# Performance work log

Hardware: AMD Instinct MI355X
Metric: run time of the kernel (lower is better)

Reference implementation:

```python
import jax, jax.numpy as jnp
import numpy as np

S, E, H, D, F = 2048, 1280, 16, 80, 5120
EPS = 1e-6


def _ln(x, g, b):
    m = x.mean(-1, keepdims=True)
    v = x.var(-1, keepdims=True)
    return (x - m) * jax.lax.rsqrt(v + EPS) * g + b


def _rotate_half(x):
    x1, x2 = jnp.split(x, 2, axis=-1)
    return jnp.concatenate([-x2, x1], axis=-1)


def _quick_gelu(x):
    return x * jax.nn.sigmoid(1.702 * x)


def setup_inputs() -> dict:
    key = jax.random.key(0)
    ks = jax.random.split(key, 12)
    inp = {
        "hidden_states": jax.random.normal(ks[0], (S, E), jnp.float32),
        "attention_mask": jnp.ones((1, 1, S, S), jnp.bool_),
        "cos": jax.random.uniform(ks[1], (S, D), jnp.float32),
        "sin": jax.random.uniform(ks[2], (S, D), jnp.float32),
        "ln1_g": jnp.ones((E,), jnp.float32),
        "ln1_b": jnp.zeros((E,), jnp.float32),
        "ln2_g": jnp.ones((E,), jnp.float32),
        "ln2_b": jnp.zeros((E,), jnp.float32),
        "w_qkv": jax.random.normal(ks[3], (E, 3 * E), jnp.float32) * (E ** -0.5),
        "b_qkv": jax.random.normal(ks[4], (3 * E,), jnp.float32) * 0.02,
        "w_o": jax.random.normal(ks[5], (E, E), jnp.float32) * (E ** -0.5),
        "b_o": jax.random.normal(ks[6], (E,), jnp.float32) * 0.02,
        "w_fc1": jax.random.normal(ks[7], (E, F), jnp.float32) * (E ** -0.5),
        "b_fc1": jax.random.normal(ks[8], (F,), jnp.float32) * 0.02,
        "w_fc2": jax.random.normal(ks[9], (F, E), jnp.float32) * (F ** -0.5),
        "b_fc2": jax.random.normal(ks[10], (E,), jnp.float32) * 0.02,
    }
    return inp


def reference(hidden_states, attention_mask, cos, sin, ln1_g, ln1_b, ln2_g, ln2_b,
              w_qkv, b_qkv, w_o, b_o, w_fc1, b_fc1, w_fc2, b_fc2):
    x = hidden_states  # [S, E]
    h = _ln(x, ln1_g, ln1_b)
    qkv = h @ w_qkv + b_qkv  # [S, 3E]
    q, k, v = jnp.split(qkv, 3, axis=-1)
    q = q.reshape(S, H, D)
    k = k.reshape(S, H, D)
    v = v.reshape(S, H, D)
    # rotary in fp32, cos/sin broadcast over head axis: [S, 1, D]
    c = cos[:, None, :].astype(jnp.float32)
    s = sin[:, None, :].astype(jnp.float32)
    qf, kf = q.astype(jnp.float32), k.astype(jnp.float32)
    q = (qf * c + _rotate_half(qf) * s).astype(q.dtype)
    k = (kf * c + _rotate_half(kf) * s).astype(k.dtype)
    # attention scores [H, S, S]
    scores = jnp.einsum('shd,thd->hst', q, k) / np.float32(np.sqrt(D))
    scores = jnp.where(attention_mask[0], scores, jnp.finfo(scores.dtype).min)
    probs = jax.nn.softmax(scores.astype(jnp.float32), axis=-1).astype(q.dtype)
    attn = jnp.einsum('hst,thd->shd', probs, v).reshape(S, E)
    attn = attn @ w_o + b_o
    x = x + attn
    h2 = _ln(x, ln2_g, ln2_b)
    mlp = _quick_gelu(h2 @ w_fc1 + b_fc1) @ w_fc2 + b_fc2
    return x + mlp
```

## Files before the change

kernel.cpp:

```cpp
#include <hip/hip_runtime.h>
#include <stdint.h>
#include <math.h>

#define S_LEN 2048
#define EMB   1280
#define NHEAD 16
#define HDIM  80
#define FDIM  5120

typedef __bf16 bf16x8 __attribute__((ext_vector_type(8)));
typedef float  f32x4  __attribute__((ext_vector_type(4)));
typedef int    i32x4  __attribute__((ext_vector_type(4)));
typedef unsigned short u16x8 __attribute__((ext_vector_type(8)));
typedef unsigned short u16x4 __attribute__((ext_vector_type(4)));

__device__ __forceinline__ float b2f(unsigned short u) {
    union { float f; unsigned int i; } x; x.i = ((unsigned int)u) << 16; return x.f;
}
__device__ __forceinline__ unsigned short f2b(float f) {
    union { float f; unsigned int i; } x; x.f = f;
    unsigned int r = x.i + 0x7FFFu + ((x.i >> 16) & 1u);
    return (unsigned short)(r >> 16);
}

__device__ __forceinline__ float wave_rsum(float v) {
    #pragma unroll
    for (int o = 32; o; o >>= 1) v += __shfl_down(v, o);
    return v;
}

typedef const __attribute__((address_space(1))) unsigned int* as1_u32p;
typedef __attribute__((address_space(3))) unsigned int* as3_u32p;
__device__ __forceinline__ void gload16(const unsigned short* g, unsigned short* l) {
    __builtin_amdgcn_global_load_lds((as1_u32p)g, (as3_u32p)l, 16, 0, 0);
}

__global__ __launch_bounds__(256) void transpose_conv_kernel(
    const float* __restrict__ in, unsigned short* __restrict__ out,
    int R, int C)
{
    __shared__ unsigned short tile[64][65];
    int c0 = blockIdx.x * 64, r0 = blockIdx.y * 64;
    int tx = threadIdx.x & 63, ty = threadIdx.x >> 6;
    #pragma unroll
    for (int j = 0; j < 16; ++j) {
        int row = ty + j * 4;
        tile[row][tx] = f2b(in[(size_t)(r0 + row) * C + c0 + tx]);
    }
    __syncthreads();
    #pragma unroll
    for (int j = 0; j < 16; ++j) {
        int row = ty + j * 4;
        out[(size_t)(c0 + row) * R + r0 + tx] = tile[tx][row];
    }
}

__global__ __launch_bounds__(256) void ln_kernel(
    const float* __restrict__ x,
    const float* __restrict__ g,
    const float* __restrict__ b,
    unsigned short* __restrict__ out)
{
    int row = blockIdx.x, tid = threadIdx.x;
    int lane = tid & 63, wave = tid >> 6;
    const float* xr = x + (size_t)row * EMB;
    float v[5], s = 0.f, ss = 0.f;
    #pragma unroll
    for (int i = 0; i < 5; ++i) {
        float f = xr[tid + i * 256];
        v[i] = f; s += f; ss += f * f;
    }
    s = wave_rsum(s); ss = wave_rsum(ss);
    __shared__ float rs[4], rss[4];
    if (lane == 0) { rs[wave] = s; rss[wave] = ss; }
    __syncthreads();
    float st  = rs[0] + rs[1] + rs[2] + rs[3];
    float sst = rss[0] + rss[1] + rss[2] + rss[3];
    float mean = st * (1.0f / EMB);
    float var  = sst * (1.0f / EMB) - mean * mean;
    float inv  = rsqrtf(var + 1e-6f);
    unsigned short* orow = out + (size_t)row * EMB;
    #pragma unroll
    for (int i = 0; i < 5; ++i) {
        int c = tid + i * 256;
        orow[c] = f2b((v[i] - mean) * inv * g[c] + b[c]);
    }
}

template<int EPI, int OM, int NT, int SPLIT>
__global__ __launch_bounds__(256) void gemm_kernel(
    const unsigned short* __restrict__ A,
    const unsigned short* __restrict__ Bt,
    const float* __restrict__ bias,
    const float* __restrict__ res,
    void* __restrict__ Cv,
    int M, int N, int K)
{
    __shared__ __align__(16) unsigned short As[128 * 32];
    __shared__ __align__(16) unsigned short Bs[NT * 32 * 32];

    int tid = threadIdx.x;
    int lane = tid & 63, wave = tid >> 6;
    int m0 = blockIdx.x * 128, n0 = blockIdx.y * (NT * 32);
    int wm = (wave >> 1) * 64, wn = (wave & 1) * (NT * 16);
    int kc = K / SPLIT;
    int kbeg = blockIdx.z * kc;

    f32x4 acc[4][NT];
    #pragma unroll
    for (int i = 0; i < 4; ++i)
        #pragma unroll
        for (int j = 0; j < NT; ++j)
            acc[i][j] = (f32x4){0.f, 0.f, 0.f, 0.f};

    int srow = tid >> 2;
    int scol = (tid & 3) * 8;
    const unsigned short* Ap0 = A  + (size_t)(m0 + srow) * K + scol + kbeg;
    const unsigned short* Ap1 = Ap0 + (size_t)64 * K;
    const unsigned short* Bp0 = Bt + (size_t)(n0 + srow) * K + scol + kbeg;
    const unsigned short* Bp1 = Bp0 + (size_t)64 * K;
    unsigned short* Asw0 = &As[srow * 32 + scol];
    unsigned short* Asw1 = &As[(srow + 64) * 32 + scol];
    unsigned short* Bsw0 = &Bs[srow * 32 + scol];
    unsigned short* Bsw1 = &Bs[(srow + 64) * 32 + scol];

    int arow = lane & 15, aq = (lane >> 4) * 8;
    int aoff[4], boff[NT];
    #pragma unroll
    for (int i = 0; i < 4; ++i)
        aoff[i] = (wm + i * 16 + arow) * 32 + aq;
    #pragma unroll
    for (int i = 0; i < NT; ++i)
        boff[i] = (wn + i * 16 + arow) * 32 + aq;

    for (int k0 = 0; k0 < kc; k0 += 32) {
        __syncthreads();
        gload16(Ap0 + k0, Asw0);
        gload16(Ap1 + k0, Asw1);
        gload16(Bp0 + k0, Bsw0);
        if (NT == 4) gload16(Bp1 + k0, Bsw1);
        __syncthreads();

        bf16x8 af[4], bfm[NT];
        #pragma unroll
        for (int i = 0; i < 4; ++i)
            af[i] = *(const bf16x8*)&As[aoff[i]];
        #pragma unroll
        for (int i = 0; i < NT; ++i)
            bfm[i] = *(const bf16x8*)&Bs[boff[i]];
        #pragma unroll
        for (int mi = 0; mi < 4; ++mi)
            #pragma unroll
            for (int ni = 0; ni < NT; ++ni)
                acc[mi][ni] = __builtin_amdgcn_mfma_f32_16x16x32_bf16(
                    af[mi], bfm[ni], acc[mi][ni], 0, 0, 0);
    }

    int col = lane & 15;
    int rbase = (lane >> 4) * 4;
    #pragma unroll
    for (int ni = 0; ni < NT; ++ni) {
        int gn = n0 + wn + ni * 16 + col;
        float bv = (OM == 2) ? 0.f : bias[gn];
        #pragma unroll
        for (int mi = 0; mi < 4; ++mi) {
            int gm = m0 + wm + mi * 16 + rbase;
            #pragma unroll
            for (int r = 0; r < 4; ++r) {
                float v = acc[mi][ni][r] + bv;
                if (OM != 2) {
                    if (EPI == 1) v = v / (1.0f + expf(-1.702f * v));
                    if (EPI == 2) v += res[(size_t)(gm + r) * N + gn];
                }
                if (OM == 2)
                    ((float*)Cv)[((size_t)blockIdx.z * M + gm + r) * N + gn] = v;
                else if (OM == 1)
                    ((float*)Cv)[(size_t)(gm + r) * N + gn] = v;
                else
                    ((unsigned short*)Cv)[(size_t)(gm + r) * N + gn] = f2b(v);
            }
        }
    }
}

__global__ __launch_bounds__(256) void reduce4_kernel(
    const float* __restrict__ part,
    const float* __restrict__ res,
    const float* __restrict__ bias,
    float* __restrict__ out)
{
    size_t i4 = ((size_t)blockIdx.x * 256 + threadIdx.x) * 4;
    int colb = (int)(i4 % EMB);
    f32x4 a = *(const f32x4*)&res[i4];
    f32x4 bv = *(const f32x4*)&bias[colb];
    a += bv;
    const size_t slice = (size_t)S_LEN * EMB;
    #pragma unroll
    for (int z = 0; z < 4; ++z)
        a += *(const f32x4*)&part[z * slice + i4];
    *(f32x4*)&out[i4] = a;
}

__global__ __launch_bounds__(128) void rope_kernel(
    const unsigned short* __restrict__ qkv,
    const float* __restrict__ cosb,
    const float* __restrict__ sinb,
    unsigned short* __restrict__ q_out,
    unsigned short* __restrict__ k_out)
{
    int bs = blockIdx.x;
    int s = bs / NHEAD, h = bs % NHEAD;
    int d = threadIdx.x;
    if (d >= HDIM) return;
    const unsigned short* base = qkv + (size_t)s * (3 * EMB) + h * HDIM;
    int partner = (d < 40) ? d + 40 : d - 40;
    float sgn = (d < 40) ? -1.f : 1.f;
    float qv = b2f(base[d]);
    float kv = b2f(base[EMB + d]);
    float qr = b2f(base[partner]) * sgn;
    float kr = b2f(base[EMB + partner]) * sgn;
    float c  = cosb[s * HDIM + d];
    float sn = sinb[s * HDIM + d];
    size_t o = ((size_t)h * S_LEN + s) * HDIM + d;
    q_out[o] = f2b(qv * c + qr * sn);
    k_out[o] = f2b(kv * c + kr * sn);
}

__global__ __launch_bounds__(256) void vtrans_kernel(
    const unsigned short* __restrict__ qkv,
    unsigned short* __restrict__ vt)
{
    __shared__ unsigned short t[64 * 84];
    int h = blockIdx.x >> 5, stile = blockIdx.x & 31;
    int s0 = stile * 64;
    int tid = threadIdx.x;
    #pragma unroll
    for (int i = 0; i < 5; ++i) {
        int u = tid + i * 256;
        int row = u / 20, col = (u % 20) * 4;
        *(u16x4*)&t[row * 84 + col] =
            *(const u16x4*)(qkv + (size_t)(s0 + row) * (3 * EMB) + 2 * EMB + h * HDIM + col);
    }
    __syncthreads();
    #pragma unroll
    for (int i = 0; i < 5; ++i) {
        int w = tid + i * 256;
        int d = w >> 4, c4 = (w & 15) * 4;
        u16x4 pk;
        #pragma unroll
        for (int j = 0; j < 4; ++j) pk[j] = t[(c4 + j) * 84 + d];
        *(u16x4*)(vt + ((size_t)h * HDIM + d) * S_LEN + s0 + c4) = pk;
    }
}

__global__ __launch_bounds__(256) void fattn_kernel(
    const unsigned short* __restrict__ q,
    const unsigned short* __restrict__ k,
    const unsigned short* __restrict__ vt,
    unsigned short* __restrict__ out)
{
    __shared__ __align__(16) unsigned short Qs[64 * 96];
    __shared__ __align__(16) unsigned short Ks[64 * 96];
    __shared__ __align__(16) unsigned short Vs[80 * 72];
    __shared__ __align__(16) unsigned short Pt[4 * 16 * 72];

    int tid = threadIdx.x;
    int lane = tid & 63, wave = tid >> 6;
    int arow = lane & 15, quad = lane >> 4;
    int h = blockIdx.x >> 5, qb = blockIdx.x & 31;
    int s0 = qb * 64;
    const float c = 0.16129856f;

    const unsigned short* qbase = q + ((size_t)h * S_LEN + s0) * HDIM;
    const unsigned short* kbase = k + (size_t)h * S_LEN * HDIM;
    const unsigned short* vbase = vt + (size_t)h * HDIM * S_LEN;

    #pragma unroll
    for (int i = 0; i < 5; ++i) {
        int u = tid + i * 256;
        int row = u / 20, col = (u % 20) * 4;
        *(u16x4*)&Qs[row * 96 + col] = *(const u16x4*)(qbase + u * 4);
    }
    {
        int zr = tid >> 2, zc = 80 + (tid & 3) * 4;
        *(u16x4*)&Qs[zr * 96 + zc] = (u16x4){0, 0, 0, 0};
        *(u16x4*)&Ks[zr * 96 + zc] = (u16x4){0, 0, 0, 0};
    }

    int pw = wave * 16 * 72;
    float m_run = -3e38f;
    float l_run = 0.f;
    f32x4 o[5];
    #pragma unroll
    for (int di = 0; di < 5; ++di) o[di] = (f32x4){0.f, 0.f, 0.f, 0.f};

    for (int it = 0; it < S_LEN / 64; ++it) {
        int t0 = it * 64;
        u16x4 kreg[5], vreg[5];
        #pragma unroll
        for (int i = 0; i < 5; ++i) {
            int u = tid + i * 256;
            kreg[i] = *(const u16x4*)(kbase + (size_t)t0 * HDIM + u * 4);
            int vrow = u >> 4, vc4 = (u & 15) * 4;
            vreg[i] = *(const u16x4*)(vbase + (size_t)vrow * S_LEN + t0 + vc4);
        }
        __syncthreads();
        #pragma unroll
        for (int i = 0; i < 5; ++i) {
            int u = tid + i * 256;
            *(u16x4*)&Ks[(u / 20) * 96 + (u % 20) * 4] = kreg[i];
            *(u16x4*)&Vs[(u >> 4) * 72 + (u & 15) * 4] = vreg[i];
        }
        __syncthreads();

        f32x4 sc[4];
        #pragma unroll
        for (int ni = 0; ni < 4; ++ni) sc[ni] = (f32x4){0.f, 0.f, 0.f, 0.f};
        #pragma unroll
        for (int kk = 0; kk < 3; ++kk) {
            bf16x8 bq = *(const bf16x8*)&Qs[(wave * 16 + arow) * 96 + kk * 32 + quad * 8];
            #pragma unroll
            for (int ni = 0; ni < 4; ++ni) {
                bf16x8 ak = *(const bf16x8*)&Ks[(ni * 16 + arow) * 96 + kk * 32 + quad * 8];
                sc[ni] = __builtin_amdgcn_mfma_f32_16x16x32_bf16(ak, bq, sc[ni], 0, 0, 0);
            }
        }

        float tm = -3e38f;
        #pragma unroll
        for (int ni = 0; ni < 4; ++ni)
            #pragma unroll
            for (int r = 0; r < 4; ++r) tm = fmaxf(tm, sc[ni][r]);
        tm = fmaxf(tm, __shfl_xor(tm, 16));
        tm = fmaxf(tm, __shfl_xor(tm, 32));
        float mn = fmaxf(m_run, tm);
        float alpha = exp2f((m_run - mn) * c);
        m_run = mn;
        float mc = mn * c;
        float rs = 0.f;
        #pragma unroll
        for (int ni = 0; ni < 4; ++ni) {
            #pragma unroll
            for (int r = 0; r < 4; ++r) {
                float p = exp2f(sc[ni][r] * c - mc);
                sc[ni][r] = p;
                rs += p;
            }
        }
        rs += __shfl_xor(rs, 16);
        rs += __shfl_xor(rs, 32);
        l_run = l_run * alpha + rs;

        #pragma unroll
        for (int ni = 0; ni < 4; ++ni) {
            u16x4 pk;
            #pragma unroll
            for (int r = 0; r < 4; ++r) {
                __bf16 pb = (__bf16)sc[ni][r];
                pk[r] = *(unsigned short*)&pb;
            }
            *(u16x4*)&Pt[pw + arow * 72 + ni * 16 + quad * 4] = pk;
        }

        float al[4];
        #pragma unroll
        for (int r = 0; r < 4; ++r)
            al[r] = __shfl(alpha, (lane & 48) | (quad * 4 + r));
        #pragma unroll
        for (int di = 0; di < 5; ++di)
            #pragma unroll
            for (int r = 0; r < 4; ++r) o[di][r] *= al[r];

        #pragma unroll
        for (int kk = 0; kk < 2; ++kk) {
            bf16x8 ap = *(const bf16x8*)&Pt[pw + arow * 72 + kk * 32 + quad * 8];
            #pragma unroll
            for (int di = 0; di < 5; ++di) {
                bf16x8 bv = *(const bf16x8*)&Vs[(di * 16 + arow) * 72 + kk * 32 + quad * 8];
                o[di] = __builtin_amdgcn_mfma_f32_16x16x32_bf16(ap, bv, o[di], 0, 0, 0);
            }
        }
    }

    float inv[4];
    #pragma unroll
    for (int r = 0; r < 4; ++r)
        inv[r] = 1.f / __shfl(l_run, (lane & 48) | (quad * 4 + r));
    #pragma unroll
    for (int r = 0; r < 4; ++r) {
        int gq = s0 + wave * 16 + quad * 4 + r;
        unsigned short* op = out + (size_t)gq * EMB + h * HDIM;
        #pragma unroll
        for (int di = 0; di < 5; ++di)
            op[di * 16 + arow] = f2b(o[di][r] * inv[r]);
    }
}

extern "C" void kernel_launch(void* const* d_in, const int* in_sizes, int n_in,
                              void* d_out, int out_size, void* d_ws, size_t ws_size,
                              hipStream_t stream)
{
    const float* hidden = (const float*)d_in[0];
    const float* cosb  = (const float*)d_in[2];
    const float* sinb  = (const float*)d_in[3];
    const float* ln1g  = (const float*)d_in[4];
    const float* ln1b  = (const float*)d_in[5];
    const float* ln2g  = (const float*)d_in[6];
    const float* ln2b  = (const float*)d_in[7];
    const float* w_qkv = (const float*)d_in[8];
    const float* b_qkv = (const float*)d_in[9];
    const float* w_o   = (const float*)d_in[10];
    const float* b_o   = (const float*)d_in[11];
    const float* w_fc1 = (const float*)d_in[12];
    const float* b_fc1 = (const float*)d_in[13];
    const float* w_fc2 = (const float*)d_in[14];
    const float* b_fc2 = (const float*)d_in[15];

    char* ws = (char*)d_ws;
    size_t off = 0;
    auto alloc = [&](size_t bytes) -> void* {
        void* p = (void*)(ws + off);
        off += (bytes + 255) & ~(size_t)255;
        return p;
    };
    unsigned short* wT_qkv = (unsigned short*)alloc((size_t)3840 * 1280 * 2);
    unsigned short* wT_o   = (unsigned short*)alloc((size_t)1280 * 1280 * 2);
    unsigned short* wT_fc1 = (unsigned short*)alloc((size_t)5120 * 1280 * 2);
    unsigned short* wT_fc2 = (unsigned short*)alloc((size_t)1280 * 5120 * 2);
    unsigned short* h1     = (unsigned short*)alloc((size_t)S_LEN * EMB * 2);
    unsigned short* qkv    = (unsigned short*)alloc((size_t)S_LEN * 3 * EMB * 2);
    unsigned short* q_r    = (unsigned short*)alloc((size_t)S_LEN * EMB * 2);
    unsigned short* k_r    = (unsigned short*)alloc((size_t)S_LEN * EMB * 2);
    unsigned short* vt_g   = (unsigned short*)alloc((size_t)S_LEN * EMB * 2);
    unsigned short* attn_o = (unsigned short*)alloc((size_t)S_LEN * EMB * 2);
    float*          x1     = (float*)alloc((size_t)S_LEN * EMB * 4);
    unsigned short* h2     = (unsigned short*)alloc((size_t)S_LEN * EMB * 2);
    unsigned short* mlp1   = (unsigned short*)alloc((size_t)S_LEN * FDIM * 2);
    float* fc2part = (float*)h1;

    transpose_conv_kernel<<<dim3(3840 / 64, 1280 / 64), 256, 0, stream>>>(w_qkv, wT_qkv, 1280, 3840);
    transpose_conv_kernel<<<dim3(1280 / 64, 1280 / 64), 256, 0, stream>>>(w_o,   wT_o,   1280, 1280);
    transpose_conv_kernel<<<dim3(5120 / 64, 1280 / 64), 256, 0, stream>>>(w_fc1, wT_fc1, 1280, 5120);
    transpose_conv_kernel<<<dim3(1280 / 64, 5120 / 64), 256, 0, stream>>>(w_fc2, wT_fc2, 5120, 1280);

    ln_kernel<<<S_LEN, 256, 0, stream>>>(hidden, ln1g, ln1b, h1);

    gemm_kernel<0, 0, 4, 1><<<dim3(S_LEN / 128, 3840 / 128, 1), 256, 0, stream>>>(
        h1, wT_qkv, b_qkv, nullptr, qkv, S_LEN, 3 * EMB, EMB);

    rope_kernel<<<S_LEN * NHEAD, 128, 0, stream>>>(qkv, cosb, sinb, q_r, k_r);
    vtrans_kernel<<<NHEAD * (S_LEN / 64), 256, 0, stream>>>(qkv, vt_g);

    fattn_kernel<<<NHEAD * (S_LEN / 64), 256, 0, stream>>>(q_r, k_r, vt_g, attn_o);

    gemm_kernel<2, 1, 2, 1><<<dim3(S_LEN / 128, 1280 / 64, 1), 256, 0, stream>>>(
        attn_o, wT_o, b_o, hidden, x1, S_LEN, EMB, EMB);

    ln_kernel<<<S_LEN, 256, 0, stream>>>(x1, ln2g, ln2b, h2);

    gemm_kernel<1, 0, 4, 1><<<dim3(S_LEN / 128, FDIM / 128, 1), 256, 0, stream>>>(
        h2, wT_fc1, b_fc1, nullptr, mlp1, S_LEN, FDIM, EMB);

    gemm_kernel<0, 2, 4, 4><<<dim3(S_LEN / 128, 1280 / 128, 4), 256, 0, stream>>>(
        mlp1, wT_fc2, b_fc2, nullptr, fc2part, S_LEN, EMB, FDIM);
    reduce4_kernel<<<(S_LEN * EMB / 4) / 256, 256, 0, stream>>>(
        fc2part, x1, b_fc2, (float*)d_out);
}
```

Before: 416.4 us.

## Double-buffer attention K/V tiles, widen GEMM K-step, fuse RoPE with V transpose

Result: faster. 406.3 us (-2.4%).

```diff
diff --git a/kernel.cpp b/kernel.cpp
--- a/kernel.cpp
+++ b/kernel.cpp
@@ -96,8 +96,8 @@
     void* __restrict__ Cv,
     int M, int N, int K)
 {
-    __shared__ __align__(16) unsigned short As[128 * 32];
-    __shared__ __align__(16) unsigned short Bs[NT * 32 * 32];
+    __shared__ __align__(16) unsigned short As[2][128 * 32];
+    __shared__ __align__(16) unsigned short Bs[2][NT * 32 * 32];
 
     int tid = threadIdx.x;
     int lane = tid & 63, wave = tid >> 6;
@@ -113,16 +113,10 @@
         for (int j = 0; j < NT; ++j)
             acc[i][j] = (f32x4){0.f, 0.f, 0.f, 0.f};
 
-    int srow = tid >> 2;
-    int scol = (tid & 3) * 8;
-    const unsigned short* Ap0 = A  + (size_t)(m0 + srow) * K + scol + kbeg;
+    const unsigned short* Ap0 = A  + (size_t)(m0 + (tid >> 2)) * K + (tid & 3) * 8 + kbeg;
     const unsigned short* Ap1 = Ap0 + (size_t)64 * K;
-    const unsigned short* Bp0 = Bt + (size_t)(n0 + srow) * K + scol + kbeg;
+    const unsigned short* Bp0 = Bt + (size_t)(n0 + (tid >> 2)) * K + (tid & 3) * 8 + kbeg;
     const unsigned short* Bp1 = Bp0 + (size_t)64 * K;
-    unsigned short* Asw0 = &As[srow * 32 + scol];
-    unsigned short* Asw1 = &As[(srow + 64) * 32 + scol];
-    unsigned short* Bsw0 = &Bs[srow * 32 + scol];
-    unsigned short* Bsw1 = &Bs[(srow + 64) * 32 + scol];
 
     int arow = lane & 15, aq = (lane >> 4) * 8;
     int aoff[4], boff[NT];
@@ -133,27 +127,34 @@
     for (int i = 0; i < NT; ++i)
         boff[i] = (wn + i * 16 + arow) * 32 + aq;
 
-    for (int k0 = 0; k0 < kc; k0 += 32) {
+    for (int k0 = 0; k0 < kc; k0 += 64) {
         __syncthreads();
-        gload16(Ap0 + k0, Asw0);
-        gload16(Ap1 + k0, Asw1);
-        gload16(Bp0 + k0, Bsw0);
-        if (NT == 4) gload16(Bp1 + k0, Bsw1);
+        gload16(Ap0 + k0,      &As[0][tid * 8]);
+        gload16(Ap1 + k0,      &As[0][2048 + tid * 8]);
+        gload16(Bp0 + k0,      &Bs[0][tid * 8]);
+        if (NT == 4) gload16(Bp1 + k0, &Bs[0][2048 + tid * 8]);
+        gload16(Ap0 + k0 + 32, &As[1][tid * 8]);
+        gload16(Ap1 + k0 + 32, &As[1][2048 + tid * 8]);
+        gload16(Bp0 + k0 + 32, &Bs[1][tid * 8]);
+        if (NT == 4) gload16(Bp1 + k0 + 32, &Bs[1][2048 + tid * 8]);
         __syncthreads();
 
-        bf16x8 af[4], bfm[NT];
-        #pragma unroll
-        for (int i = 0; i < 4; ++i)
-            af[i] = *(const bf16x8*)&As[aoff[i]];
-        #pragma unroll
-        for (int i = 0; i < NT; ++i)
-            bfm[i] = *(const bf16x8*)&Bs[boff[i]];
-        #pragma unroll
-        for (int mi = 0; mi < 4; ++mi)
-            #pragma unroll
-            for (int ni = 0; ni < NT; ++ni)
-                acc[mi][ni] = __builtin_amdgcn_mfma_f32_16x16x32_bf16(
-                    af[mi], bfm[ni], acc[mi][ni], 0, 0, 0);
+        #pragma unroll
+        for (int p = 0; p < 2; ++p) {
+            bf16x8 af[4], bfm[NT];
+            #pragma unroll
+            for (int i = 0; i < 4; ++i)
+                af[i] = *(const bf16x8*)&As[p][aoff[i]];
+            #pragma unroll
+            for (int i = 0; i < NT; ++i)
+                bfm[i] = *(const bf16x8*)&Bs[p][boff[i]];
+            #pragma unroll
+            for (int mi = 0; mi < 4; ++mi)
+                #pragma unroll
+                for (int ni = 0; ni < NT; ++ni)
+                    acc[mi][ni] = __builtin_amdgcn_mfma_f32_16x16x32_bf16(
+                        af[mi], bfm[ni], acc[mi][ni], 0, 0, 0);
+        }
     }
 
     int col = lane & 15;
@@ -201,55 +202,65 @@
     *(f32x4*)&out[i4] = a;
 }
 
-__global__ __launch_bounds__(128) void rope_kernel(
+__global__ __launch_bounds__(256) void ropev_kernel(
     const unsigned short* __restrict__ qkv,
     const float* __restrict__ cosb,
     const float* __restrict__ sinb,
     unsigned short* __restrict__ q_out,
-    unsigned short* __restrict__ k_out)
-{
-    int bs = blockIdx.x;
-    int s = bs / NHEAD, h = bs % NHEAD;
-    int d = threadIdx.x;
-    if (d >= HDIM) return;
-    const unsigned short* base = qkv + (size_t)s * (3 * EMB) + h * HDIM;
-    int partner = (d < 40) ? d + 40 : d - 40;
-    float sgn = (d < 40) ? -1.f : 1.f;
-    float qv = b2f(base[d]);
-    float kv = b2f(base[EMB + d]);
-    float qr = b2f(base[partner]) * sgn;
-    float kr = b2f(base[EMB + partner]) * sgn;
-    float c  = cosb[s * HDIM + d];
-    float sn = sinb[s * HDIM + d];
-    size_t o = ((size_t)h * S_LEN + s) * HDIM + d;
-    q_out[o] = f2b(qv * c + qr * sn);
-    k_out[o] = f2b(kv * c + kr * sn);
-}
-
-__global__ __launch_bounds__(256) void vtrans_kernel(
-    const unsigned short* __restrict__ qkv,
+    unsigned short* __restrict__ k_out,
     unsigned short* __restrict__ vt)
 {
-    __shared__ unsigned short t[64 * 84];
+    __shared__ unsigned short qT[64 * 84];
+    __shared__ unsigned short kT[64 * 84];
+    __shared__ unsigned short vT[64 * 84];
+
     int h = blockIdx.x >> 5, stile = blockIdx.x & 31;
     int s0 = stile * 64;
     int tid = threadIdx.x;
+
+    u16x4 qr[5], kr[5];
     #pragma unroll
     for (int i = 0; i < 5; ++i) {
         int u = tid + i * 256;
         int row = u / 20, col = (u % 20) * 4;
-        *(u16x4*)&t[row * 84 + col] =
-            *(const u16x4*)(qkv + (size_t)(s0 + row) * (3 * EMB) + 2 * EMB + h * HDIM + col);
+        const unsigned short* base = qkv + (size_t)(s0 + row) * (3 * EMB) + h * HDIM + col;
+        qr[i] = *(const u16x4*)base;
+        kr[i] = *(const u16x4*)(base + EMB);
+        u16x4 v4 = *(const u16x4*)(base + 2 * EMB);
+        *(u16x4*)&qT[row * 84 + col] = qr[i];
+        *(u16x4*)&kT[row * 84 + col] = kr[i];
+        *(u16x4*)&vT[row * 84 + col] = v4;
     }
     __syncthreads();
+
+    #pragma unroll
+    for (int i = 0; i < 5; ++i) {
+        int u = tid + i * 256;
+        int row = u / 20, col = (u % 20) * 4;
+        int pcol = (col < 40) ? col + 40 : col - 40;
+        float sgn = (col < 40) ? -1.f : 1.f;
+        u16x4 qp = *(const u16x4*)&qT[row * 84 + pcol];
+        u16x4 kp = *(const u16x4*)&kT[row * 84 + pcol];
+        f32x4 c4 = *(const f32x4*)&cosb[(size_t)(s0 + row) * HDIM + col];
+        f32x4 s4 = *(const f32x4*)&sinb[(size_t)(s0 + row) * HDIM + col];
+        u16x4 qo, ko;
+        #pragma unroll
+        for (int j = 0; j < 4; ++j) {
+            qo[j] = f2b(b2f(qr[i][j]) * c4[j] + sgn * b2f(qp[j]) * s4[j]);
+            ko[j] = f2b(b2f(kr[i][j]) * c4[j] + sgn * b2f(kp[j]) * s4[j]);
+        }
+        size_t o = ((size_t)h * S_LEN + s0 + row) * HDIM + col;
+        *(u16x4*)&q_out[o] = qo;
+        *(u16x4*)&k_out[o] = ko;
+    }
     #pragma unroll
     for (int i = 0; i < 5; ++i) {
         int w = tid + i * 256;
-        int d = w >> 4, c4 = (w & 15) * 4;
+        int d = w >> 4, c4i = (w & 15) * 4;
         u16x4 pk;
         #pragma unroll
-        for (int j = 0; j < 4; ++j) pk[j] = t[(c4 + j) * 84 + d];
-        *(u16x4*)(vt + ((size_t)h * HDIM + d) * S_LEN + s0 + c4) = pk;
+        for (int j = 0; j < 4; ++j) pk[j] = vT[(c4i + j) * 84 + d];
+        *(u16x4*)(vt + ((size_t)h * HDIM + d) * S_LEN + s0 + c4i) = pk;
     }
 }
 
@@ -260,8 +271,8 @@
     unsigned short* __restrict__ out)
 {
     __shared__ __align__(16) unsigned short Qs[64 * 96];
-    __shared__ __align__(16) unsigned short Ks[64 * 96];
-    __shared__ __align__(16) unsigned short Vs[80 * 72];
+    __shared__ __align__(16) unsigned short Ks[2][64 * 96];
+    __shared__ __align__(16) unsigned short Vs[2][80 * 72];
     __shared__ __align__(16) unsigned short Pt[4 * 16 * 72];
 
     int tid = threadIdx.x;
@@ -283,9 +294,31 @@
     }
     {
         int zr = tid >> 2, zc = 80 + (tid & 3) * 4;
-        *(u16x4*)&Qs[zr * 96 + zc] = (u16x4){0, 0, 0, 0};
-        *(u16x4*)&Ks[zr * 96 + zc] = (u16x4){0, 0, 0, 0};
-    }
+        *(u16x4*)&Qs[zr * 96 + zc]    = (u16x4){0, 0, 0, 0};
+        *(u16x4*)&Ks[0][zr * 96 + zc] = (u16x4){0, 0, 0, 0};
+        *(u16x4*)&Ks[1][zr * 96 + zc] = (u16x4){0, 0, 0, 0};
+    }
+
+    u16x4 kreg[5], vreg[5];
+    #pragma unroll
+    for (int i = 0; i < 5; ++i) {
+        int u = tid + i * 256;
+        kreg[i] = *(const u16x4*)(kbase + u * 4);
+        vreg[i] = *(const u16x4*)(vbase + (size_t)(u >> 4) * S_LEN + (u & 15) * 4);
+    }
+    #pragma unroll
+    for (int i = 0; i < 5; ++i) {
+        int u = tid + i * 256;
+        *(u16x4*)&Ks[0][(u / 20) * 96 + (u % 20) * 4] = kreg[i];
+        *(u16x4*)&Vs[0][(u >> 4) * 72 + (u & 15) * 4] = vreg[i];
+    }
+    #pragma unroll
+    for (int i = 0; i < 5; ++i) {
+        int u = tid + i * 256;
+        kreg[i] = *(const u16x4*)(kbase + (size_t)64 * HDIM + u * 4);
+        vreg[i] = *(const u16x4*)(vbase + (size_t)(u >> 4) * S_LEN + 64 + (u & 15) * 4);
+    }
+    __syncthreads();
 
     int pw = wave * 16 * 72;
     float m_run = -3e38f;
@@ -294,24 +327,27 @@
     #pragma unroll
     for (int di = 0; di < 5; ++di) o[di] = (f32x4){0.f, 0.f, 0.f, 0.f};
 
-    for (int it = 0; it < S_LEN / 64; ++it) {
-        int t0 = it * 64;
-        u16x4 kreg[5], vreg[5];
-        #pragma unroll
-        for (int i = 0; i < 5; ++i) {
-            int u = tid + i * 256;
-            kreg[i] = *(const u16x4*)(kbase + (size_t)t0 * HDIM + u * 4);
-            int vrow = u >> 4, vc4 = (u & 15) * 4;
-            vreg[i] = *(const u16x4*)(vbase + (size_t)vrow * S_LEN + t0 + vc4);
-        }
-        __syncthreads();
-        #pragma unroll
-        for (int i = 0; i < 5; ++i) {
-            int u = tid + i * 256;
-            *(u16x4*)&Ks[(u / 20) * 96 + (u % 20) * 4] = kreg[i];
-            *(u16x4*)&Vs[(u >> 4) * 72 + (u & 15) * 4] = vreg[i];
-        }
-        __syncthreads();
+    const int NIT = S_LEN / 64;
+    for (int it = 0; it < NIT; ++it) {
+        int cur = it & 1;
+        if (it + 1 < NIT) {
+            int nb = (it + 1) & 1;
+            #pragma unroll
+            for (int i = 0; i < 5; ++i) {
+                int u = tid + i * 256;
+                *(u16x4*)&Ks[nb][(u / 20) * 96 + (u % 20) * 4] = kreg[i];
+                *(u16x4*)&Vs[nb][(u >> 4) * 72 + (u & 15) * 4] = vreg[i];
+            }
+        }
+        if (it + 2 < NIT) {
+            int t0 = (it + 2) * 64;
+            #pragma unroll
+            for (int i = 0; i < 5; ++i) {
+                int u = tid + i * 256;
+                kreg[i] = *(const u16x4*)(kbase + (size_t)t0 * HDIM + u * 4);
+                vreg[i] = *(const u16x4*)(vbase + (size_t)(u >> 4) * S_LEN + t0 + (u & 15) * 4);
+            }
+        }
 
         f32x4 sc[4];
         #pragma unroll
@@ -321,7 +357,7 @@
             bf16x8 bq = *(const bf16x8*)&Qs[(wave * 16 + arow) * 96 + kk * 32 + quad * 8];
             #pragma unroll
             for (int ni = 0; ni < 4; ++ni) {
-                bf16x8 ak = *(const bf16x8*)&Ks[(ni * 16 + arow) * 96 + kk * 32 + quad * 8];
+                bf16x8 ak = *(const bf16x8*)&Ks[cur][(ni * 16 + arow) * 96 + kk * 32 + quad * 8];
                 sc[ni] = __builtin_amdgcn_mfma_f32_16x16x32_bf16(ak, bq, sc[ni], 0, 0, 0);
             }
         }
@@ -376,10 +412,12 @@
             bf16x8 ap = *(const bf16x8*)&Pt[pw + arow * 72 + kk * 32 + quad * 8];
             #pragma unroll
             for (int di = 0; di < 5; ++di) {
-                bf16x8 bv = *(const bf16x8*)&Vs[(di * 16 + arow) * 72 + kk * 32 + quad * 8];
+                bf16x8 bv = *(const bf16x8*)&Vs[cur][(di * 16 + arow) * 72 + kk * 32 + quad * 8];
                 o[di] = __builtin_amdgcn_mfma_f32_16x16x32_bf16(ap, bv, o[di], 0, 0, 0);
             }
         }
+
+        __syncthreads();
     }
 
     float inv[4];
@@ -448,8 +486,7 @@
     gemm_kernel<0, 0, 4, 1><<<dim3(S_LEN / 128, 3840 / 128, 1), 256, 0, stream>>>(
         h1, wT_qkv, b_qkv, nullptr, qkv, S_LEN, 3 * EMB, EMB);
 
-    rope_kernel<<<S_LEN * NHEAD, 128, 0, stream>>>(qkv, cosb, sinb, q_r, k_r);
-    vtrans_kernel<<<NHEAD * (S_LEN / 64), 256, 0, stream>>>(qkv, vt_g);
+    ropev_kernel<<<NHEAD * (S_LEN / 64), 256, 0, stream>>>(qkv, cosb, sinb, q_r, k_r, vt_g);
 
     fattn_kernel<<<NHEAD * (S_LEN / 64), 256, 0, stream>>>(q_r, k_r, vt_g, attn_o);
 
```
